# Kernel tuning notes

Hardware: AMD Instinct MI355X
Metric: run time of the kernel (lower is better)

## Reference

```python
import jax, jax.numpy as jnp
import numpy as np

BIG_NUMBER = 1000000.0
B, N, H = 8, 256, 128   # batch, nodes, node/hidden feat
E, G = 128, 128         # edge feat, graph feat
MID, OUT = 128, 128
IN_Z = 2 * H


def setup_inputs() -> dict:
    key = jax.random.key(0)
    ks = jax.random.split(key, 20)
    sc = lambda fan_in: 1.0 / np.sqrt(fan_in)
    inp = {
        "node_fts": jax.random.normal(ks[0], (B, N, H), jnp.float32),
        "edge_fts": jax.random.normal(ks[1], (B, N, N, E), jnp.float32),
        "graph_fts": jax.random.normal(ks[2], (B, G), jnp.float32),
        "adj_mat": (jax.random.uniform(ks[3], (B, N, N)) < 0.5).astype(jnp.float32),
        "hidden": jax.random.normal(ks[4], (B, N, H), jnp.float32),
        # linear params, stored [in, out]
        "W1": jax.random.normal(ks[5], (IN_Z, MID), jnp.float32) * sc(IN_Z),
        "b1": jnp.zeros((MID,), jnp.float32),
        "W2": jax.random.normal(ks[6], (IN_Z, MID), jnp.float32) * sc(IN_Z),
        "b2": jnp.zeros((MID,), jnp.float32),
        "We": jax.random.normal(ks[7], (E, MID), jnp.float32) * sc(E),
        "be": jnp.zeros((MID,), jnp.float32),
        "Wg": jax.random.normal(ks[8], (G, MID), jnp.float32) * sc(G),
        "bg": jnp.zeros((MID,), jnp.float32),
        "Wo1": jax.random.normal(ks[9], (IN_Z, OUT), jnp.float32) * sc(IN_Z),
        "bo1": jnp.zeros((OUT,), jnp.float32),
        "Wo2": jax.random.normal(ks[10], (MID, OUT), jnp.float32) * sc(MID),
        "bo2": jnp.zeros((OUT,), jnp.float32),
    }
    return inp


def reference(node_fts, edge_fts, graph_fts, adj_mat, hidden,
              W1, b1, W2, b2, We, be, Wg, bg, Wo1, bo1, Wo2, bo2):
    # z: [b, n, 2h]
    z = jnp.concatenate([node_fts, hidden], axis=-1)
    msg_1 = z @ W1 + b1                       # [b, n, mid]
    msg_2 = z @ W2 + b2                       # [b, n, mid]
    msg_e = edge_fts @ We + be                # [b, n, n, mid]
    msg_g = graph_fts @ Wg + bg               # [b, mid]
    # msgs[b, i, j, :]; reduce over i (senders)
    msgs = (msg_1[:, None, :, :] + msg_2[:, :, None, :]
            + msg_e + msg_g[:, None, None, :])
    maxarg = jnp.where(adj_mat[..., None] > 0, msgs, -BIG_NUMBER)
    msgs_red = jnp.max(maxarg, axis=1)        # [b, n, mid]
    ret = jax.nn.relu((z @ Wo1 + bo1) + (msgs_red @ Wo2 + bo2))
    return ret
```

## Files before the change

### kernel.cpp

```cpp
#include <hip/hip_runtime.h>
#include <hip/hip_bf16.h>
#include <stdint.h>
#include <stddef.h>

#define B_   8
#define N_   256
#define H_   128
#define E_   128
#define INZ  256
#define BIGN 1000000.0f

typedef float f32x4 __attribute__((ext_vector_type(4)));
typedef short bf16x8 __attribute__((ext_vector_type(8)));

static __device__ __forceinline__ unsigned cvt2(float a, float b) {
    unsigned short ra = __builtin_bit_cast(unsigned short, __float2bfloat16(a));
    unsigned short rb = __builtin_bit_cast(unsigned short, __float2bfloat16(b));
    return (unsigned)ra | ((unsigned)rb << 16);
}

static __device__ __forceinline__ bf16x8 mk_frag(f32x4 lo, f32x4 h4) {
    union { unsigned u[4]; bf16x8 v; } r;
    r.u[0] = cvt2(lo.x, lo.y);
    r.u[1] = cvt2(lo.z, lo.w);
    r.u[2] = cvt2(h4.x, h4.y);
    r.u[3] = cvt2(h4.z, h4.w);
    return r.v;
}

__global__ __launch_bounds__(256) void prep_kernel(
    const float* __restrict__ node, const float* __restrict__ hidden,
    const float* __restrict__ gf,
    const float* __restrict__ W1, const float* __restrict__ b1,
    const float* __restrict__ W2, const float* __restrict__ b2,
    const float* __restrict__ Wg, const float* __restrict__ bg,
    const float* __restrict__ Wo1, const float* __restrict__ bo1,
    const float* __restrict__ We,
    float* __restrict__ msg1, float* __restrict__ m2g,
    float* __restrict__ zo1, unsigned short* __restrict__ weT)
{
    __shared__ float zs[4][INZ];
    const int t  = threadIdx.x;
    const int r0 = blockIdx.x * 4;
    const int b  = r0 >> 8;

    for (int idx = t; idx < 4 * INZ; idx += 256) {
        int r = idx >> 8, k = idx & 255;
        int row = r0 + r;
        zs[r][k] = (k < H_) ? node[(size_t)row * H_ + k]
                            : hidden[(size_t)row * H_ + (k - H_)];
    }
    if (blockIdx.x < 8) {
        int e0 = blockIdx.x * 2048;
        for (int e = e0 + t; e < e0 + 2048; e += 256) {
            int n = e >> 7, k = e & 127;
            weT[e] = (unsigned short)__builtin_bit_cast(unsigned short,
                         __float2bfloat16(We[k * 128 + n]));
        }
    }
    __syncthreads();

    const int col = t & 127;
    const int rg  = t >> 7;
    float a1[2] = {0, 0}, a2[2] = {0, 0}, ao[2] = {0, 0};

#pragma unroll 4
    for (int k = 0; k < INZ; ++k) {
        float w1 = W1[k * 128 + col];
        float w2 = W2[k * 128 + col];
        float wo = Wo1[k * 128 + col];
#pragma unroll
        for (int rr = 0; rr < 2; ++rr) {
            float zv = zs[rg * 2 + rr][k];
            a1[rr] = fmaf(zv, w1, a1[rr]);
            a2[rr] = fmaf(zv, w2, a2[rr]);
            ao[rr] = fmaf(zv, wo, ao[rr]);
        }
    }
    float mg = bg[col];
#pragma unroll 4
    for (int g = 0; g < 128; ++g)
        mg = fmaf(gf[b * 128 + g], Wg[g * 128 + col], mg);

    const float bb1 = b1[col], bb2 = b2[col], bbo = bo1[col];
#pragma unroll
    for (int rr = 0; rr < 2; ++rr) {
        size_t row = (size_t)(r0 + rg * 2 + rr);
        msg1[row * 128 + col] = a1[rr] + bb1;
        m2g[row * 128 + col]  = a2[rr] + bb2 + mg;
        zo1[row * 128 + col]  = ao[rr] + bbo;
    }
}

__global__ __launch_bounds__(256, 2) void pgn_main(
    const float* __restrict__ edge, const float* __restrict__ adj,
    const float* __restrict__ m2g, const unsigned short* __restrict__ weT,
    float* __restrict__ redp)
{
    const int t    = threadIdx.x;
    const int lane = t & 63, wid = t >> 6;
    const int hi   = lane >> 4, c15 = lane & 15;
    const int blk  = blockIdx.x;
    const int b    = blk >> 6;
    const int ic   = (blk >> 2) & 15;
    const int jq   = blk & 3;
    const int i0   = ic * 16;
    const int jrow = jq * 64 + wid * 16 + c15;

    bf16x8 bfr[8][4];
#pragma unroll
    for (int n = 0; n < 8; ++n) {
#pragma unroll
        for (int ks = 0; ks < 4; ++ks)
            bfr[n][ks] = *(const bf16x8*)(weT + (n * 16 + c15) * 128 + ks * 32 + hi * 8);
    }

    float rmax[8][4];
#pragma unroll
    for (int n = 0; n < 8; ++n)
#pragma unroll
        for (int rg = 0; rg < 4; ++rg) rmax[n][rg] = -BIGN;

    const float* abase = edge + ((size_t)(b * N_ + i0) * N_ + jrow) * E_ + hi * 8;
    const float* adjb  = adj + (size_t)(b * N_ + i0) * N_ + jq * 64 + wid * 16 + hi * 4;
    const float* m2gb  = m2g + (size_t)(b * N_ + i0) * 128 + c15;

#pragma unroll 2
    for (int ii = 0; ii < 16; ++ii) {
        const float* ar = abase + (size_t)ii * (N_ * E_);

        f32x4 a4 = *(const f32x4*)(adjb + (size_t)ii * N_);
        float mv[8];
#pragma unroll
        for (int n = 0; n < 8; ++n) mv[n] = m2gb[(size_t)ii * 128 + n * 16];

        f32x4 acc[8] = {};
#pragma unroll
        for (int ks = 0; ks < 4; ++ks) {
            f32x4 lo = *(const f32x4*)(ar + ks * 32);
            f32x4 h4 = *(const f32x4*)(ar + ks * 32 + 4);
            bf16x8 af = mk_frag(lo, h4);
#pragma unroll
            for (int n = 0; n < 8; ++n)
                acc[n] = __builtin_amdgcn_mfma_f32_16x16x32_bf16(
                    af, bfr[n][ks], acc[n], 0, 0, 0);
        }

#pragma unroll
        for (int n = 0; n < 8; ++n)
#pragma unroll
            for (int rg = 0; rg < 4; ++rg) {
                float v = acc[n][rg] + mv[n];
                v = (a4[rg] > 0.0f) ? v : -BIGN;
                rmax[n][rg] = fmaxf(rmax[n][rg], v);
            }
    }

    float* rp = redp + (size_t)blk * 8192;
#pragma unroll
    for (int n = 0; n < 8; ++n)
#pragma unroll
        for (int rg = 0; rg < 4; ++rg) {
            int jl = wid * 16 + hi * 4 + rg;
            rp[jl * 128 + n * 16 + c15] = rmax[n][rg];
        }
}

__global__ __launch_bounds__(256) void finish_kernel(
    const float* __restrict__ redp, const float* __restrict__ msg1,
    const float* __restrict__ zo1, const float* __restrict__ be,
    const float* __restrict__ Wo2, const float* __restrict__ bo2,
    float* __restrict__ out)
{
    __shared__ float rb[8][128];
    const int t  = threadIdx.x;
    const int r0 = blockIdx.x * 8;

    for (int idx = t; idx < 1024; idx += 256) {
        int rr = idx >> 7, k = idx & 127;
        int r  = r0 + rr;
        int b  = r >> 8, j = r & 255;
        int jq = j >> 6, jl = j & 63;
        float v = -BIGN - 1.0f;
#pragma unroll 4
        for (int ic = 0; ic < 16; ++ic)
            v = fmaxf(v, redp[(size_t)(((b * 16 + ic) * 4) + jq) * 8192 + jl * 128 + k]);
        rb[rr][k] = v + msg1[(size_t)r * 128 + k] + be[k];
    }
    __syncthreads();

    const int col  = t & 127;
    const int half = t >> 7;
#pragma unroll
    for (int rx = 0; rx < 4; ++rx) {
        int rr = half * 4 + rx;
        size_t row = (size_t)(r0 + rr);
        float a = 0.0f;
#pragma unroll 8
        for (int k = 0; k < 128; ++k)
            a = fmaf(rb[rr][k], Wo2[k * 128 + col], a);
        float o = zo1[row * 128 + col] + bo2[col] + a;
        out[row * 128 + col] = fmaxf(o, 0.0f);
    }
}

extern "C" void kernel_launch(void* const* d_in, const int* in_sizes, int n_in,
                              void* d_out, int out_size, void* d_ws, size_t ws_size,
                              hipStream_t stream) {
    const float* node   = (const float*)d_in[0];
    const float* edge   = (const float*)d_in[1];
    const float* gf     = (const float*)d_in[2];
    const float* adj    = (const float*)d_in[3];
    const float* hidden = (const float*)d_in[4];
    const float* W1  = (const float*)d_in[5];
    const float* b1  = (const float*)d_in[6];
    const float* W2  = (const float*)d_in[7];
    const float* b2  = (const float*)d_in[8];
    const float* We  = (const float*)d_in[9];
    const float* be  = (const float*)d_in[10];
    const float* Wg  = (const float*)d_in[11];
    const float* bg  = (const float*)d_in[12];
    const float* Wo1 = (const float*)d_in[13];
    const float* bo1 = (const float*)d_in[14];
    const float* Wo2 = (const float*)d_in[15];
    const float* bo2 = (const float*)d_in[16];
    float* out = (float*)d_out;

    float* msg1 = (float*)d_ws;
    float* m2g  = msg1 + 2048 * 128;
    float* zo1  = m2g + 2048 * 128;
    unsigned short* weT = (unsigned short*)(zo1 + 2048 * 128);
    float* redp = (float*)((char*)weT + 128 * 128 * sizeof(unsigned short));

    hipLaunchKernelGGL(prep_kernel, dim3(512), dim3(256), 0, stream,
                       node, hidden, gf, W1, b1, W2, b2, Wg, bg, Wo1, bo1, We,
                       msg1, m2g, zo1, weT);
    hipLaunchKernelGGL(pgn_main, dim3(512), dim3(256), 0, stream,
                       edge, adj, m2g, weT, redp);
    hipLaunchKernelGGL(finish_kernel, dim3(256), dim3(256), 0, stream,
                       redp, msg1, zo1, be, Wo2, bo2, out);
}
```

Before: 120.3 us.

## Stage We in swizzled LDS, prefetch edge rows, split senders finer

The transposed bf16 We matrix is written in an XOR-swizzled layout and copied into shared memory per block, so B fragments are read from LDS instead of being held in 128 registers. This is meant to raise occupancy (launch bounds 2→3). Edge loads for an iteration are now issued together before conversion. When the workspace is large enough, the sender dimension is split into 32 chunks instead of 16, doubling the grid to expose more parallelism. The cost is more partial-max traffic for the finish kernel and LDS read pressure in the MFMA loop.

```diff
diff --git a/kernel.cpp b/kernel.cpp
--- a/kernel.cpp
+++ b/kernel.cpp
@@ -54,8 +54,9 @@
         int e0 = blockIdx.x * 2048;
         for (int e = e0 + t; e < e0 + 2048; e += 256) {
             int n = e >> 7, k = e & 127;
-            weT[e] = (unsigned short)__builtin_bit_cast(unsigned short,
-                         __float2bfloat16(We[k * 128 + n]));
+            weT[(n * 128 + k) ^ ((n & 7) << 3)] =
+                (unsigned short)__builtin_bit_cast(unsigned short,
+                    __float2bfloat16(We[k * 128 + n]));
         }
     }
     __syncthreads();
@@ -92,27 +93,29 @@
     }
 }
 
-__global__ __launch_bounds__(256, 2) void pgn_main(
+__global__ __launch_bounds__(256, 3) void pgn_main(
     const float* __restrict__ edge, const float* __restrict__ adj,
     const float* __restrict__ m2g, const unsigned short* __restrict__ weT,
-    float* __restrict__ redp)
+    float* __restrict__ redp, int icbits)
 {
+    __shared__ __align__(16) short blds[128 * 128];
+
     const int t    = threadIdx.x;
     const int lane = t & 63, wid = t >> 6;
     const int hi   = lane >> 4, c15 = lane & 15;
     const int blk  = blockIdx.x;
-    const int b    = blk >> 6;
-    const int ic   = (blk >> 2) & 15;
     const int jq   = blk & 3;
-    const int i0   = ic * 16;
+    const int ic   = (blk >> 2) & ((1 << icbits) - 1);
+    const int b    = blk >> (icbits + 2);
+    const int ni   = N_ >> icbits;
+    const int i0   = ic * ni;
     const int jrow = jq * 64 + wid * 16 + c15;
 
-    bf16x8 bfr[8][4];
-#pragma unroll
-    for (int n = 0; n < 8; ++n) {
-#pragma unroll
-        for (int ks = 0; ks < 4; ++ks)
-            bfr[n][ks] = *(const bf16x8*)(weT + (n * 16 + c15) * 128 + ks * 32 + hi * 8);
+    {
+        const uint4* ws = (const uint4*)weT;
+        uint4* wd = (uint4*)blds;
+#pragma unroll
+        for (int q = 0; q < 8; ++q) wd[t + 256 * q] = ws[t + 256 * q];
     }
 
     float rmax[8][4];
@@ -125,10 +128,27 @@
     const float* adjb  = adj + (size_t)(b * N_ + i0) * N_ + jq * 64 + wid * 16 + hi * 4;
     const float* m2gb  = m2g + (size_t)(b * N_ + i0) * 128 + c15;
 
+    int boff[8][4];
+#pragma unroll
+    for (int n = 0; n < 8; ++n) {
+        int rowB = n * 16 + c15;
+#pragma unroll
+        for (int ks = 0; ks < 4; ++ks)
+            boff[n][ks] = (rowB * 256 + ks * 64 + hi * 16) ^ ((rowB & 7) << 4);
+    }
+
+    __syncthreads();
+
 #pragma unroll 2
-    for (int ii = 0; ii < 16; ++ii) {
+    for (int ii = 0; ii < ni; ++ii) {
         const float* ar = abase + (size_t)ii * (N_ * E_);
 
+        f32x4 pf[8];
+#pragma unroll
+        for (int ks = 0; ks < 4; ++ks) {
+            pf[2 * ks]     = *(const f32x4*)(ar + ks * 32);
+            pf[2 * ks + 1] = *(const f32x4*)(ar + ks * 32 + 4);
+        }
         f32x4 a4 = *(const f32x4*)(adjb + (size_t)ii * N_);
         float mv[8];
 #pragma unroll
@@ -137,13 +157,13 @@
         f32x4 acc[8] = {};
 #pragma unroll
         for (int ks = 0; ks < 4; ++ks) {
-            f32x4 lo = *(const f32x4*)(ar + ks * 32);
-            f32x4 h4 = *(const f32x4*)(ar + ks * 32 + 4);
-            bf16x8 af = mk_frag(lo, h4);
-#pragma unroll
-            for (int n = 0; n < 8; ++n)
+            bf16x8 af = mk_frag(pf[2 * ks], pf[2 * ks + 1]);
+#pragma unroll
+            for (int n = 0; n < 8; ++n) {
+                bf16x8 bv = *(const bf16x8*)((const char*)blds + boff[n][ks]);
                 acc[n] = __builtin_amdgcn_mfma_f32_16x16x32_bf16(
-                    af, bfr[n][ks], acc[n], 0, 0, 0);
+                    af, bv, acc[n], 0, 0, 0);
+            }
         }
 
 #pragma unroll
@@ -170,11 +190,12 @@
     const float* __restrict__ redp, const float* __restrict__ msg1,
     const float* __restrict__ zo1, const float* __restrict__ be,
     const float* __restrict__ Wo2, const float* __restrict__ bo2,
-    float* __restrict__ out)
+    float* __restrict__ out, int icbits)
 {
     __shared__ float rb[8][128];
     const int t  = threadIdx.x;
     const int r0 = blockIdx.x * 8;
+    const int S  = 1 << icbits;
 
     for (int idx = t; idx < 1024; idx += 256) {
         int rr = idx >> 7, k = idx & 127;
@@ -182,9 +203,9 @@
         int b  = r >> 8, j = r & 255;
         int jq = j >> 6, jl = j & 63;
         float v = -BIGN - 1.0f;
-#pragma unroll 4
-        for (int ic = 0; ic < 16; ++ic)
-            v = fmaxf(v, redp[(size_t)(((b * 16 + ic) * 4) + jq) * 8192 + jl * 128 + k]);
+        for (int p = 0; p < S; ++p)
+            v = fmaxf(v, redp[(size_t)(((b << icbits) + p) * 4 + jq) * 8192
+                              + jl * 128 + k]);
         rb[rr][k] = v + msg1[(size_t)r * 128 + k] + be[k];
     }
     __syncthreads();
@@ -232,11 +253,15 @@
     unsigned short* weT = (unsigned short*)(zo1 + 2048 * 128);
     float* redp = (float*)((char*)weT + 128 * 128 * sizeof(unsigned short));
 
+    const size_t fixed = 3u * 1048576u + 32768u;
+    int icbits = (ws_size >= fixed + 33u * 1048576u) ? 5 : 4;
+    int nblk   = 32 << icbits;
+
     hipLaunchKernelGGL(prep_kernel, dim3(512), dim3(256), 0, stream,
                        node, hidden, gf, W1, b1, W2, b2, Wg, bg, Wo1, bo1, We,
                        msg1, m2g, zo1, weT);
-    hipLaunchKernelGGL(pgn_main, dim3(512), dim3(256), 0, stream,
-                       edge, adj, m2g, weT, redp);
+    hipLaunchKernelGGL(pgn_main, dim3(nblk), dim3(256), 0, stream,
+                       edge, adj, m2g, weT, redp, icbits);
     hipLaunchKernelGGL(finish_kernel, dim3(256), dim3(256), 0, stream,
-                       redp, msg1, zo1, be, Wo2, bo2, out);
-}
+                       redp, msg1, zo1, be, Wo2, bo2, out, icbits);
+}
```

Result: slower. 231.8 us (+92.7%).

## Stage edge tiles through swizzled LDS with register prefetch, split output columns across waves

Applied to the files above, without the earlier changes.

The main kernel now loads each pair of sender rows cooperatively with coalesced 16-byte loads, converts them to bf16 and stores them into an XOR-swizzled LDS tile. The next pair is prefetched into registers while MFMAs run on the current one. Each wave now owns 32 output columns instead of all 128, which cuts register use so occupancy can rise to 4 blocks per SIMD. Grid size and the partial-max count depend on workspace size, so the finish kernel reads a variable number of partials. The cost is two barriers per iteration and more, smaller blocks.

```diff
diff --git a/kernel.cpp b/kernel.cpp
--- a/kernel.cpp
+++ b/kernel.cpp
@@ -17,15 +17,6 @@
     unsigned short ra = __builtin_bit_cast(unsigned short, __float2bfloat16(a));
     unsigned short rb = __builtin_bit_cast(unsigned short, __float2bfloat16(b));
     return (unsigned)ra | ((unsigned)rb << 16);
-}
-
-static __device__ __forceinline__ bf16x8 mk_frag(f32x4 lo, f32x4 h4) {
-    union { unsigned u[4]; bf16x8 v; } r;
-    r.u[0] = cvt2(lo.x, lo.y);
-    r.u[1] = cvt2(lo.z, lo.w);
-    r.u[2] = cvt2(h4.x, h4.y);
-    r.u[3] = cvt2(h4.z, h4.w);
-    return r.v;
 }
 
 __global__ __launch_bounds__(256) void prep_kernel(
@@ -92,99 +83,142 @@
     }
 }
 
-__global__ __launch_bounds__(256, 2) void pgn_main(
+__global__ __launch_bounds__(256, 4) void pgn_main(
     const float* __restrict__ edge, const float* __restrict__ adj,
     const float* __restrict__ m2g, const unsigned short* __restrict__ weT,
-    float* __restrict__ redp)
+    float* __restrict__ redp, int icsbits)
 {
+    __shared__ __align__(16) char atile[8192];
+
     const int t    = threadIdx.x;
-    const int lane = t & 63, wid = t >> 6;
+    const int lane = t & 63, w = t >> 6;
     const int hi   = lane >> 4, c15 = lane & 15;
     const int blk  = blockIdx.x;
-    const int b    = blk >> 6;
-    const int ic   = (blk >> 2) & 15;
-    const int jq   = blk & 3;
-    const int i0   = ic * 16;
-    const int jrow = jq * 64 + wid * 16 + c15;
-
-    bf16x8 bfr[8][4];
-#pragma unroll
-    for (int n = 0; n < 8; ++n) {
+    const int jt   = blk & 15;
+    const int ICS  = 1 << icsbits;
+    const int ic   = (blk >> 4) & (ICS - 1);
+    const int b    = blk >> (4 + icsbits);
+    const int j0   = jt * 16;
+    const int ni   = N_ >> icsbits;
+    const int NT   = ni >> 1;
+    const int i0   = ic * ni;
+
+    bf16x8 bfr[2][4];
+#pragma unroll
+    for (int nn = 0; nn < 2; ++nn) {
+        int ecol = w * 32 + nn * 16 + c15;
 #pragma unroll
         for (int ks = 0; ks < 4; ++ks)
-            bfr[n][ks] = *(const bf16x8*)(weT + (n * 16 + c15) * 128 + ks * 32 + hi * 8);
-    }
-
-    float rmax[8][4];
-#pragma unroll
-    for (int n = 0; n < 8; ++n)
-#pragma unroll
-        for (int rg = 0; rg < 4; ++rg) rmax[n][rg] = -BIGN;
-
-    const float* abase = edge + ((size_t)(b * N_ + i0) * N_ + jrow) * E_ + hi * 8;
-    const float* adjb  = adj + (size_t)(b * N_ + i0) * N_ + jq * 64 + wid * 16 + hi * 4;
-    const float* m2gb  = m2g + (size_t)(b * N_ + i0) * 128 + c15;
-
-#pragma unroll 2
-    for (int ii = 0; ii < 16; ++ii) {
-        const float* ar = abase + (size_t)ii * (N_ * E_);
-
-        f32x4 a4 = *(const f32x4*)(adjb + (size_t)ii * N_);
-        float mv[8];
-#pragma unroll
-        for (int n = 0; n < 8; ++n) mv[n] = m2gb[(size_t)ii * 128 + n * 16];
-
-        f32x4 acc[8] = {};
+            bfr[nn][ks] = *(const bf16x8*)(weT + ecol * 128 + ks * 32 + hi * 8);
+    }
+
+    const float* gp[4];
+    int lo[4];
+#pragma unroll
+    for (int r = 0; r < 4; ++r) {
+        int q = r * 256 + t;
+        int di = q >> 9, rowj = (q >> 5) & 15, qr = q & 31;
+        gp[r] = edge + (((size_t)(b * N_ + i0 + di)) * N_ + (j0 + rowj)) * E_ + qr * 4;
+        lo[r] = di * 4096 + rowj * 256 + ((qr * 8) ^ ((rowj & 7) << 4));
+    }
+    const size_t tstep = (size_t)2 * N_ * E_;
+
+    f32x4 ld[4];
+#pragma unroll
+    for (int r = 0; r < 4; ++r) ld[r] = *(const f32x4*)(gp[r]);
+
+    float rmax[2][4];
+#pragma unroll
+    for (int nn = 0; nn < 2; ++nn)
+#pragma unroll
+        for (int rg = 0; rg < 4; ++rg) rmax[nn][rg] = -BIGN;
+
+    for (int tt = 0; tt < NT; ++tt) {
+        asm volatile("s_waitcnt lgkmcnt(0)" ::: "memory");
+        __builtin_amdgcn_s_barrier();
+        __builtin_amdgcn_sched_barrier(0);
+
+#pragma unroll
+        for (int r = 0; r < 4; ++r) {
+            uint2 s;
+            s.x = cvt2(ld[r].x, ld[r].y);
+            s.y = cvt2(ld[r].z, ld[r].w);
+            *(uint2*)(atile + lo[r]) = s;
+        }
+        asm volatile("s_waitcnt lgkmcnt(0)" ::: "memory");
+        __builtin_amdgcn_s_barrier();
+        __builtin_amdgcn_sched_barrier(0);
+
+        const int ib = b * N_ + i0 + 2 * tt;
+        f32x4 aj0 = *(const f32x4*)(adj + (size_t)ib * N_ + j0 + hi * 4);
+        f32x4 aj1 = *(const f32x4*)(adj + (size_t)(ib + 1) * N_ + j0 + hi * 4);
+        float mv00 = m2g[(size_t)ib * 128 + w * 32 + c15];
+        float mv01 = m2g[(size_t)ib * 128 + w * 32 + 16 + c15];
+        float mv10 = m2g[(size_t)(ib + 1) * 128 + w * 32 + c15];
+        float mv11 = m2g[(size_t)(ib + 1) * 128 + w * 32 + 16 + c15];
+        if (tt + 1 < NT) {
+#pragma unroll
+            for (int r = 0; r < 4; ++r)
+                ld[r] = *(const f32x4*)(gp[r] + (size_t)(tt + 1) * tstep);
+        }
+
+        f32x4 acc[2][2] = {};
 #pragma unroll
         for (int ks = 0; ks < 4; ++ks) {
-            f32x4 lo = *(const f32x4*)(ar + ks * 32);
-            f32x4 h4 = *(const f32x4*)(ar + ks * 32 + 4);
-            bf16x8 af = mk_frag(lo, h4);
-#pragma unroll
-            for (int n = 0; n < 8; ++n)
-                acc[n] = __builtin_amdgcn_mfma_f32_16x16x32_bf16(
-                    af, bfr[n][ks], acc[n], 0, 0, 0);
-        }
-
-#pragma unroll
-        for (int n = 0; n < 8; ++n)
+            int ko = (ks * 64 + hi * 16) ^ ((c15 & 7) << 4);
+            bf16x8 a0 = *(const bf16x8*)(atile + c15 * 256 + ko);
+            bf16x8 a1 = *(const bf16x8*)(atile + 4096 + c15 * 256 + ko);
+#pragma unroll
+            for (int nn = 0; nn < 2; ++nn) {
+                acc[0][nn] = __builtin_amdgcn_mfma_f32_16x16x32_bf16(
+                    a0, bfr[nn][ks], acc[0][nn], 0, 0, 0);
+                acc[1][nn] = __builtin_amdgcn_mfma_f32_16x16x32_bf16(
+                    a1, bfr[nn][ks], acc[1][nn], 0, 0, 0);
+            }
+        }
+
+#pragma unroll
+        for (int nn = 0; nn < 2; ++nn) {
+            float m0 = nn ? mv01 : mv00;
+            float m1 = nn ? mv11 : mv10;
 #pragma unroll
             for (int rg = 0; rg < 4; ++rg) {
-                float v = acc[n][rg] + mv[n];
-                v = (a4[rg] > 0.0f) ? v : -BIGN;
-                rmax[n][rg] = fmaxf(rmax[n][rg], v);
+                float v0 = acc[0][nn][rg] + m0;
+                v0 = (aj0[rg] > 0.0f) ? v0 : -BIGN;
+                float v1 = acc[1][nn][rg] + m1;
+                v1 = (aj1[rg] > 0.0f) ? v1 : -BIGN;
+                rmax[nn][rg] = fmaxf(rmax[nn][rg], fmaxf(v0, v1));
             }
-    }
-
-    float* rp = redp + (size_t)blk * 8192;
-#pragma unroll
-    for (int n = 0; n < 8; ++n)
-#pragma unroll
-        for (int rg = 0; rg < 4; ++rg) {
-            int jl = wid * 16 + hi * 4 + rg;
-            rp[jl * 128 + n * 16 + c15] = rmax[n][rg];
-        }
+        }
+    }
+
+    float* rp = redp + (size_t)blk * 2048;
+#pragma unroll
+    for (int nn = 0; nn < 2; ++nn)
+#pragma unroll
+        for (int rg = 0; rg < 4; ++rg)
+            rp[(hi * 4 + rg) * 128 + w * 32 + nn * 16 + c15] = rmax[nn][rg];
 }
 
 __global__ __launch_bounds__(256) void finish_kernel(
     const float* __restrict__ redp, const float* __restrict__ msg1,
     const float* __restrict__ zo1, const float* __restrict__ be,
     const float* __restrict__ Wo2, const float* __restrict__ bo2,
-    float* __restrict__ out)
+    float* __restrict__ out, int icsbits)
 {
     __shared__ float rb[8][128];
     const int t  = threadIdx.x;
     const int r0 = blockIdx.x * 8;
+    const int S  = 1 << icsbits;
 
     for (int idx = t; idx < 1024; idx += 256) {
         int rr = idx >> 7, k = idx & 127;
         int r  = r0 + rr;
         int b  = r >> 8, j = r & 255;
-        int jq = j >> 6, jl = j & 63;
         float v = -BIGN - 1.0f;
-#pragma unroll 4
-        for (int ic = 0; ic < 16; ++ic)
-            v = fmaxf(v, redp[(size_t)(((b * 16 + ic) * 4) + jq) * 8192 + jl * 128 + k]);
+        for (int p = 0; p < S; ++p)
+            v = fmaxf(v, redp[(size_t)((((b << icsbits) + p) << 4) + (j >> 4)) * 2048
+                              + (j & 15) * 128 + k]);
         rb[rr][k] = v + msg1[(size_t)r * 128 + k] + be[k];
     }
     __syncthreads();
@@ -232,11 +266,15 @@
     unsigned short* weT = (unsigned short*)(zo1 + 2048 * 128);
     float* redp = (float*)((char*)weT + 128 * 128 * sizeof(unsigned short));
 
+    const size_t fixed = 3u * 1048576u + 32768u;
+    int icsbits = (ws_size >= fixed + 17u * 1048576u) ? 4 : 3;
+    int nblk    = (8 * 16) << icsbits;
+
     hipLaunchKernelGGL(prep_kernel, dim3(512), dim3(256), 0, stream,
                        node, hidden, gf, W1, b1, W2, b2, Wg, bg, Wo1, bo1, We,
                        msg1, m2g, zo1, weT);
-    hipLaunchKernelGGL(pgn_main, dim3(512), dim3(256), 0, stream,
-                       edge, adj, m2g, weT, redp);
+    hipLaunchKernelGGL(pgn_main, dim3(nblk), dim3(256), 0, stream,
+                       edge, adj, m2g, weT, redp, icsbits);
     hipLaunchKernelGGL(finish_kernel, dim3(256), dim3(256), 0, stream,
-                       redp, msg1, zo1, be, Wo2, bo2, out);
-}
+                       redp, msg1, zo1, be, Wo2, bo2, out, icsbits);
+}
```

Measured after the change: 107.2 us. 1.12x faster.

## Compact adjacency per receiver and load only edge rows of present senders

Applied to the files above, without the earlier changes.

The main kernel is reorganised so each wavefront owns one receiver j and half the senders. It ballots the adjacency column into a bitmask and gathers only the edge rows whose adjacency is nonzero, in chunks of 16 with double-buffered prefetch, so masked edges are never read from memory. The bf16 We matrix is staged once per block into an XOR-swizzled shared-memory tile instead of living in registers, which frees registers for three blocks per CU. The cross-block partial max shrinks to two halves, and the finish kernel leaves fully masked rows at the -BIG sentinel to match the reference. In exchange, the kernel now does serial bitmask extraction per lane, gathers rows less regularly, and its cost depends on how dense the adjacency is.

```diff
diff --git a/kernel.cpp b/kernel.cpp
--- a/kernel.cpp
+++ b/kernel.cpp
@@ -54,8 +54,9 @@
         int e0 = blockIdx.x * 2048;
         for (int e = e0 + t; e < e0 + 2048; e += 256) {
             int n = e >> 7, k = e & 127;
-            weT[e] = (unsigned short)__builtin_bit_cast(unsigned short,
-                         __float2bfloat16(We[k * 128 + n]));
+            weT[(n * 128 + k) ^ ((n & 7) << 3)] =
+                (unsigned short)__builtin_bit_cast(unsigned short,
+                    __float2bfloat16(We[k * 128 + n]));
         }
     }
     __syncthreads();
@@ -92,78 +93,125 @@
     }
 }
 
-__global__ __launch_bounds__(256, 2) void pgn_main(
+__global__ __launch_bounds__(256, 3) void pgn_main(
     const float* __restrict__ edge, const float* __restrict__ adj,
     const float* __restrict__ m2g, const unsigned short* __restrict__ weT,
     float* __restrict__ redp)
 {
+    __shared__ __align__(16) short blds[128 * 128];
+
     const int t    = threadIdx.x;
-    const int lane = t & 63, wid = t >> 6;
+    const int lane = t & 63, w = t >> 6;
     const int hi   = lane >> 4, c15 = lane & 15;
-    const int blk  = blockIdx.x;
-    const int b    = blk >> 6;
-    const int ic   = (blk >> 2) & 15;
-    const int jq   = blk & 3;
-    const int i0   = ic * 16;
-    const int jrow = jq * 64 + wid * 16 + c15;
-
-    bf16x8 bfr[8][4];
+    const int task = blockIdx.x * 4 + w;
+    const int ih   = task & 1;
+    const int j    = (task >> 1) & 255;
+    const int b    = task >> 9;
+    const int ibase = ih * 128;
+
+    {
+        const uint4* ws = (const uint4*)weT;
+        uint4* wd = (uint4*)blds;
+#pragma unroll
+        for (int q = 0; q < 8; ++q) wd[t + 256 * q] = ws[t + 256 * q];
+    }
+    __syncthreads();
+
+    const float* ac = adj + ((size_t)(b * N_ + ibase)) * N_ + j;
+    unsigned long long m0 = __ballot(ac[(size_t)lane * N_] > 0.0f);
+    unsigned long long m1 = __ballot(ac[(size_t)(lane + 64) * N_] > 0.0f);
+    const int cnt = __popcll(m0) + __popcll(m1);
+
+    const float* erow = edge + (((size_t)(b * N_ + ibase)) * N_ + j) * E_;
+    const float* mrow = m2g + (size_t)(b * N_ + ibase) * 128;
+
+    float rmax[8];
+#pragma unroll
+    for (int n = 0; n < 8; ++n) rmax[n] = -BIGN;
+
+#define EXTRACT(MYIA, I0, I1, I2, I3)                                        \
+    {   MYIA = 0; I0 = 0; I1 = 0; I2 = 0; I3 = 0;                            \
+        _Pragma("unroll")                                                    \
+        for (int r = 0; r < 16; ++r) {                                       \
+            int ir = 0;                                                      \
+            if (m0) { ir = __builtin_ctzll(m0); m0 &= m0 - 1; }              \
+            else if (m1) { ir = 64 + __builtin_ctzll(m1); m1 &= m1 - 1; }    \
+            if (r == c15) MYIA = ir;                                         \
+            if ((r >> 2) == hi) {                                            \
+                if ((r & 3) == 0) I0 = ir;                                   \
+                else if ((r & 3) == 1) I1 = ir;                              \
+                else if ((r & 3) == 2) I2 = ir;                              \
+                else I3 = ir;                                                \
+            }                                                                \
+        }                                                                    \
+    }
+
+#define ISSUEA(PF, MYIA)                                                     \
+    {   const float* ar_ = erow + (size_t)(MYIA) * (N_ * E_) + hi * 8;       \
+        _Pragma("unroll")                                                    \
+        for (int ks = 0; ks < 4; ++ks) {                                     \
+            PF[2 * ks]     = *(const f32x4*)(ar_ + ks * 32);                 \
+            PF[2 * ks + 1] = *(const f32x4*)(ar_ + ks * 32 + 4);             \
+        }                                                                    \
+    }
+
+#define COMPUTE(PF, I0, I1, I2, I3, REM)                                     \
+    {   f32x4 acc[8] = {};                                                   \
+        _Pragma("unroll")                                                    \
+        for (int ks = 0; ks < 4; ++ks) {                                     \
+            bf16x8 af = mk_frag(PF[2 * ks], PF[2 * ks + 1]);                 \
+            _Pragma("unroll")                                                \
+            for (int n = 0; n < 8; ++n) {                                    \
+                int ecol = n * 16 + c15;                                     \
+                int ba = (ecol * 256 + ks * 64 + hi * 16) ^ ((ecol & 7) << 4);\
+                bf16x8 bv = *(const bf16x8*)((const char*)blds + ba);        \
+                acc[n] = __builtin_amdgcn_mfma_f32_16x16x32_bf16(            \
+                    af, bv, acc[n], 0, 0, 0);                                \
+            }                                                                \
+        }                                                                    \
+        _Pragma("unroll")                                                    \
+        for (int n = 0; n < 8; ++n) {                                        \
+            float v0 = acc[n][0] + mrow[(size_t)(I0) * 128 + n * 16 + c15];  \
+            float v1 = acc[n][1] + mrow[(size_t)(I1) * 128 + n * 16 + c15];  \
+            float v2 = acc[n][2] + mrow[(size_t)(I2) * 128 + n * 16 + c15];  \
+            float v3 = acc[n][3] + mrow[(size_t)(I3) * 128 + n * 16 + c15];  \
+            if (hi * 4 + 0 >= (REM)) v0 = -BIGN;                             \
+            if (hi * 4 + 1 >= (REM)) v1 = -BIGN;                             \
+            if (hi * 4 + 2 >= (REM)) v2 = -BIGN;                             \
+            if (hi * 4 + 3 >= (REM)) v3 = -BIGN;                             \
+            rmax[n] = fmaxf(rmax[n], fmaxf(fmaxf(v0, v1), fmaxf(v2, v3)));   \
+        }                                                                    \
+    }
+
+    const int nch = (cnt + 15) >> 4;
+    if (nch > 0) {
+        int iaA, a0, a1, a2, a3, iaB, b0, b1, b2, b3;
+        f32x4 pA[8], pB[8];
+        EXTRACT(iaA, a0, a1, a2, a3);
+        ISSUEA(pA, iaA);
+        int ch = 0;
+        while (true) {
+            if (ch + 1 < nch) { EXTRACT(iaB, b0, b1, b2, b3); ISSUEA(pB, iaB); }
+            COMPUTE(pA, a0, a1, a2, a3, cnt - ch * 16);
+            if (++ch >= nch) break;
+            if (ch + 1 < nch) { EXTRACT(iaA, a0, a1, a2, a3); ISSUEA(pA, iaA); }
+            COMPUTE(pB, b0, b1, b2, b3, cnt - ch * 16);
+            if (++ch >= nch) break;
+        }
+    }
+
 #pragma unroll
     for (int n = 0; n < 8; ++n) {
-#pragma unroll
-        for (int ks = 0; ks < 4; ++ks)
-            bfr[n][ks] = *(const bf16x8*)(weT + (n * 16 + c15) * 128 + ks * 32 + hi * 8);
-    }
-
-    float rmax[8][4];
-#pragma unroll
-    for (int n = 0; n < 8; ++n)
-#pragma unroll
-        for (int rg = 0; rg < 4; ++rg) rmax[n][rg] = -BIGN;
-
-    const float* abase = edge + ((size_t)(b * N_ + i0) * N_ + jrow) * E_ + hi * 8;
-    const float* adjb  = adj + (size_t)(b * N_ + i0) * N_ + jq * 64 + wid * 16 + hi * 4;
-    const float* m2gb  = m2g + (size_t)(b * N_ + i0) * 128 + c15;
-
-#pragma unroll 2
-    for (int ii = 0; ii < 16; ++ii) {
-        const float* ar = abase + (size_t)ii * (N_ * E_);
-
-        f32x4 a4 = *(const f32x4*)(adjb + (size_t)ii * N_);
-        float mv[8];
-#pragma unroll
-        for (int n = 0; n < 8; ++n) mv[n] = m2gb[(size_t)ii * 128 + n * 16];
-
-        f32x4 acc[8] = {};
-#pragma unroll
-        for (int ks = 0; ks < 4; ++ks) {
-            f32x4 lo = *(const f32x4*)(ar + ks * 32);
-            f32x4 h4 = *(const f32x4*)(ar + ks * 32 + 4);
-            bf16x8 af = mk_frag(lo, h4);
-#pragma unroll
-            for (int n = 0; n < 8; ++n)
-                acc[n] = __builtin_amdgcn_mfma_f32_16x16x32_bf16(
-                    af, bfr[n][ks], acc[n], 0, 0, 0);
-        }
-
-#pragma unroll
-        for (int n = 0; n < 8; ++n)
-#pragma unroll
-            for (int rg = 0; rg < 4; ++rg) {
-                float v = acc[n][rg] + mv[n];
-                v = (a4[rg] > 0.0f) ? v : -BIGN;
-                rmax[n][rg] = fmaxf(rmax[n][rg], v);
-            }
-    }
-
-    float* rp = redp + (size_t)blk * 8192;
-#pragma unroll
-    for (int n = 0; n < 8; ++n)
-#pragma unroll
-        for (int rg = 0; rg < 4; ++rg) {
-            int jl = wid * 16 + hi * 4 + rg;
-            rp[jl * 128 + n * 16 + c15] = rmax[n][rg];
-        }
+        float v = rmax[n];
+        v = fmaxf(v, __shfl_xor(v, 16, 64));
+        v = fmaxf(v, __shfl_xor(v, 32, 64));
+        rmax[n] = v;
+    }
+    if (hi == 0) {
+        float* rp = redp + ((size_t)(b * N_ + j) * 2 + ih) * 128;
+#pragma unroll
+        for (int n = 0; n < 8; ++n) rp[n * 16 + c15] = rmax[n];
+    }
 }
 
 __global__ __launch_bounds__(256) void finish_kernel(
@@ -179,13 +227,9 @@
     for (int idx = t; idx < 1024; idx += 256) {
         int rr = idx >> 7, k = idx & 127;
         int r  = r0 + rr;
-        int b  = r >> 8, j = r & 255;
-        int jq = j >> 6, jl = j & 63;
-        float v = -BIGN - 1.0f;
-#pragma unroll 4
-        for (int ic = 0; ic < 16; ++ic)
-            v = fmaxf(v, redp[(size_t)(((b * 16 + ic) * 4) + jq) * 8192 + jl * 128 + k]);
-        rb[rr][k] = v + msg1[(size_t)r * 128 + k] + be[k];
+        float v = fmaxf(redp[(size_t)r * 256 + k], redp[(size_t)r * 256 + 128 + k]);
+        rb[rr][k] = (v < -9.0e5f) ? v
+                                  : v + msg1[(size_t)r * 128 + k] + be[k];
     }
     __syncthreads();
 
@@ -235,7 +279,7 @@
     hipLaunchKernelGGL(prep_kernel, dim3(512), dim3(256), 0, stream,
                        node, hidden, gf, W1, b1, W2, b2, Wg, bg, Wo1, bo1, We,
                        msg1, m2g, zo1, weT);
-    hipLaunchKernelGGL(pgn_main, dim3(512), dim3(256), 0, stream,
+    hipLaunchKernelGGL(pgn_main, dim3(1024), dim3(256), 0, stream,
                        edge, adj, m2g, weT, redp);
     hipLaunchKernelGGL(finish_kernel, dim3(256), dim3(256), 0, stream,
                        redp, msg1, zo1, be, Wo2, bo2, out);
```

New measurement: 230.6 us. 91.7% more time.
